# Kernel tuning notes

Hardware: AMD Instinct MI355X
Metric: run time of the kernel (lower is better)

Reference implementation:

```python
import jax, jax.numpy as jnp
import numpy as np

N = 6000
E = 192000
H = 128
NUM_HEADS = 4

def _segsum(x, idx, n):
    return jax.ops.segment_sum(x, idx, num_segments=n)

def _gcn_encode(x, edges, W0, b0, Ws, bs):
    n = x.shape[0]
    sl = jnp.arange(n, dtype=edges.dtype)
    row = jnp.concatenate([edges[0], sl])  # source
    col = jnp.concatenate([edges[1], sl])  # target (aggregation)
    deg = _segsum(jnp.ones_like(col, dtype=x.dtype), col, n)
    dinv = jax.lax.rsqrt(deg)  # deg >= 1 thanks to self loops
    norm = (dinv[row] * dinv[col])[:, None]
    def layer(h, W, b):
        hw = h @ W
        agg = _segsum(hw[row] * norm, col, n)
        return jax.nn.relu(agg + b)
    h = layer(x, W0, b0)
    for i in range(Ws.shape[0]):
        h = layer(h, Ws[i], bs[i])
    return h

def setup_inputs() -> dict:
    key = jax.random.key(0)
    ks = jax.random.split(key, 24)
    def lin(k, fan_in, shape):
        return jax.random.normal(k, shape, dtype=jnp.float32) / np.sqrt(fan_in)
    return {
        'x_resting': jax.random.normal(ks[0], (N, 3), dtype=jnp.float32),
        'x_rigid': jax.random.normal(ks[1], (N, 3), dtype=jnp.float32),
        'edge_resting': jax.random.randint(ks[2], (2, E), 0, N, dtype=jnp.int32),
        'edge_rigid': jax.random.randint(ks[3], (2, E), 0, N, dtype=jnp.int32),
        'Wr0': lin(ks[4], 3, (3, H)), 'br0': jnp.zeros((H,), jnp.float32),
        'Wr': lin(ks[5], H, (2, H, H)), 'br': jnp.zeros((2, H), jnp.float32),
        'Wg0': lin(ks[6], 3, (3, H)), 'bg0': jnp.zeros((H,), jnp.float32),
        'Wg': lin(ks[7], H, (2, H, H)), 'bg': jnp.zeros((2, H), jnp.float32),
        'Wa': lin(ks[8], H, (NUM_HEADS, H, H)), 'ba': jnp.zeros((NUM_HEADS, H), jnp.float32),
        'Wd0': lin(ks[9], H * (NUM_HEADS + 1), (H * (NUM_HEADS + 1), H)), 'bd0': jnp.zeros((H,), jnp.float32),
        'Wd': lin(ks[10], H, (2, H, H)), 'bd': jnp.zeros((2, H), jnp.float32),
        'Wout': lin(ks[11], H, (H, 3)), 'bout': jnp.zeros((3,), jnp.float32),
    }

def reference(x_resting, x_rigid, edge_resting, edge_rigid,
              Wr0, br0, Wr, br, Wg0, bg0, Wg, bg,
              Wa, ba, Wd0, bd0, Wd, bd, Wout, bout):
    xr = _gcn_encode(x_resting, edge_resting, Wr0, br0, Wr, br)  # (N,H)
    xg = _gcn_encode(x_rigid, edge_rigid, Wg0, bg0, Wg, bg)      # (N,H)

    def head(W, b):
        q = xr @ W + b            # (N,H)
        k = xg @ W + b            # (N,H)
        attn = jax.nn.softmax(q @ k.T, axis=-1)  # (N,N) dense per head
        return attn @ xg          # (N,H)
    heads = jax.vmap(head)(Wa, ba)                       # (heads,N,H)
    pooled = heads.transpose(1, 0, 2).reshape(xr.shape[0], -1)  # (N, heads*H)

    h = jnp.concatenate([xr, pooled], axis=-1)  # (N, H*(heads+1))
    h = jax.nn.relu(h @ Wd0 + bd0)
    for i in range(Wd.shape[0]):
        h = jax.nn.relu(h @ Wd[i] + bd[i])
    return h @ Wout + bout  # (N, 3) deformed positions
```

## Files before the change

kernel.cpp:

```cpp
#include <hip/hip_runtime.h>
#include <math.h>

#define N_NODES 6000
#define N_EDGES 192000
#define H 128
#define NHEADS 4
#define HCAT 640
#define NPAD 6016
#define NTILES 188

typedef unsigned short ushort_t;
typedef __attribute__((ext_vector_type(8))) short short8;
typedef __attribute__((ext_vector_type(16))) float f32x16;

__device__ __forceinline__ void bf16split(float x, ushort_t& hi, ushort_t& lo) {
    unsigned ub = __float_as_uint(x);
    unsigned hb = ub & 0xffff0000u;
    float l = x - __uint_as_float(hb);
    hi = (ushort_t)(hb >> 16);
    lo = (ushort_t)(__float_as_uint(l) >> 16);
}

__device__ __forceinline__ void gll16(const ushort_t* g, ushort_t* l) {
    __builtin_amdgcn_global_load_lds((const __attribute__((address_space(1))) void*)g,
                                     (__attribute__((address_space(3))) void*)l, 16, 0, 0);
}

__global__ void zero_ints(int* p, int n) {
    int i = blockIdx.x * 256 + threadIdx.x;
    if (i < n) p[i] = 0;
}

__global__ void hist2(const int* __restrict__ eA, const int* __restrict__ eB,
                      int* __restrict__ cnt) {
    int e = blockIdx.x * 256 + threadIdx.x;
    int z = blockIdx.y;
    const int* edges = z ? eB : eA;
    if (e < N_EDGES) atomicAdd(&cnt[z * N_NODES + edges[N_EDGES + e]], 1);
}

__global__ __launch_bounds__(1024)
void scan2(const int* __restrict__ cnt_all, int* __restrict__ rs_all,
           float* __restrict__ dinv_all) {
    __shared__ int ps[1024];
    int z = blockIdx.x;
    const int* cnt = cnt_all + z * N_NODES;
    int* row_start = rs_all + z * (N_NODES + 1);
    float* dinv = dinv_all + z * N_NODES;
    int t = threadIdx.x;
    int base = t * 6;
    int local[6];
    int s = 0;
#pragma unroll
    for (int j = 0; j < 6; ++j) {
        int idx = base + j;
        int v = (idx < N_NODES) ? cnt[idx] : 0;
        local[j] = s;
        s += v;
        if (idx < N_NODES) dinv[idx] = rsqrtf((float)(v + 1));
    }
    ps[t] = s;
    __syncthreads();
    for (int off = 1; off < 1024; off <<= 1) {
        int v = (t >= off) ? ps[t - off] : 0;
        __syncthreads();
        ps[t] += v;
        __syncthreads();
    }
    int ex = (t > 0) ? ps[t - 1] : 0;
#pragma unroll
    for (int j = 0; j < 6; ++j) {
        int idx = base + j;
        if (idx < N_NODES) row_start[idx] = ex + local[j];
    }
    if (t == 1023) row_start[N_NODES] = ps[1023];
}

__global__ void place2(const int* __restrict__ eA, const int* __restrict__ eB,
                       const int* __restrict__ rs_all, int* __restrict__ cur_all,
                       int* __restrict__ eslot_all) {
    int e = blockIdx.x * 256 + threadIdx.x;
    int z = blockIdx.y;
    const int* edges = z ? eB : eA;
    if (e < N_EDGES) {
        int tg = edges[N_EDGES + e];
        int p = atomicAdd(&cur_all[z * N_NODES + tg], 1);
        eslot_all[(size_t)z * N_EDGES + rs_all[z * (N_NODES + 1) + tg] + p] = e;
    }
}

__global__ __launch_bounds__(256)
void gather_x3(const float* __restrict__ xA, const float* __restrict__ xB,
               const int* __restrict__ eA, const int* __restrict__ eB,
               const int* __restrict__ eslot_all, const int* __restrict__ rs_all,
               const float* __restrict__ dinv_all,
               float* __restrict__ outA, float* __restrict__ outB) {
    int z = blockIdx.y;
    int n = blockIdx.x * 256 + threadIdx.x;
    if (n >= N_NODES) return;
    const int* edges = z ? eB : eA;
    const int* eslot = eslot_all + (size_t)z * N_EDGES;
    const int* row_start = rs_all + z * (N_NODES + 1);
    const float* x = z ? xB : xA;
    const float* dv = dinv_all + z * N_NODES;
    float* out = z ? outB : outA;
    float di = dv[n];
    float a0 = x[n * 3 + 0] * di * di;
    float a1 = x[n * 3 + 1] * di * di;
    float a2 = x[n * 3 + 2] * di * di;
    int s0 = row_start[n], s1 = row_start[n + 1];
    for (int i = s0; i < s1; ++i) {
        int e = eslot[i];
        int s = edges[e];
        float nr = dv[s] * di;
        a0 += x[s * 3 + 0] * nr;
        a1 += x[s * 3 + 1] * nr;
        a2 += x[s * 3 + 2] * nr;
    }
    out[n * 3 + 0] = a0; out[n * 3 + 1] = a1; out[n * 3 + 2] = a2;
}

__global__ __launch_bounds__(256)
void gcn_gemm2(const float* __restrict__ hinA, const float* __restrict__ hinB,
               const float* __restrict__ WA, const float* __restrict__ WB,
               float* __restrict__ hwA, float* __restrict__ hwB, int in_dim,
               const float* __restrict__ bA, const float* __restrict__ bB, int do_relu) {
    __shared__ float xs[16 * H];
    int z = blockIdx.y;
    const float* hin = z ? hinB : hinA;
    const float* W = z ? WB : WA;
    float* hw = z ? hwB : hwA;
    const float* b = z ? bB : bA;
    int n0 = blockIdx.x * 16;
    int t = threadIdx.x;
    int f = t & (H - 1);
    int g = t >> 7;
    for (int i = t; i < 16 * H; i += 256) {
        int r = i >> 7, c = i & (H - 1);
        xs[i] = (c < in_dim) ? hin[(size_t)(n0 + r) * in_dim + c] : 0.f;
    }
    __syncthreads();
    float acc[8];
#pragma unroll
    for (int j = 0; j < 8; ++j) acc[j] = 0.f;
    for (int d = 0; d < in_dim; ++d) {
        float w = W[d * H + f];
#pragma unroll
        for (int j = 0; j < 8; ++j) acc[j] += xs[(g * 8 + j) * H + d] * w;
    }
    if (do_relu) {
        float bias = b[f];
#pragma unroll
        for (int j = 0; j < 8; ++j)
            hw[(size_t)(n0 + g * 8 + j) * H + f] = fmaxf(acc[j] + bias, 0.f);
    } else {
#pragma unroll
        for (int j = 0; j < 8; ++j) hw[(size_t)(n0 + g * 8 + j) * H + f] = acc[j];
    }
}

__global__ __launch_bounds__(H)
void gather2(const int* __restrict__ eA, const int* __restrict__ eB,
             const int* __restrict__ eslot_all, const int* __restrict__ rs_all,
             const float* __restrict__ hwA, const float* __restrict__ hwB,
             const float* __restrict__ dinv_all,
             const float* __restrict__ bA, const float* __restrict__ bB,
             float* __restrict__ outA, float* __restrict__ outB, int osA, int osB) {
    __shared__ int ssrc[128];
    __shared__ float snrm[128];
    int z = blockIdx.y;
    const int* edges = z ? eB : eA;
    const int* eslot = eslot_all + (size_t)z * N_EDGES;
    const int* row_start = rs_all + z * (N_NODES + 1);
    const float* hw = z ? hwB : hwA;
    const float* dinv = dinv_all + z * N_NODES;
    const float* b = z ? bB : bA;
    float* out = z ? outB : outA;
    int ostride = z ? osB : osA;

    int tg = blockIdx.x, f = threadIdx.x;
    int s0 = row_start[tg], s1 = row_start[tg + 1];
    float di = dinv[tg];
    float acc = hw[(size_t)tg * H + f] * di * di;
    for (int base = s0; base < s1; base += 128) {
        int cnt = min(128, s1 - base);
        __syncthreads();
        if (f < cnt) {
            int e = eslot[base + f];
            int s = edges[e];
            ssrc[f] = s;
            snrm[f] = dinv[s] * di;
        }
        __syncthreads();
        for (int i = 0; i < cnt; ++i)
            acc += hw[(size_t)ssrc[i] * H + f] * snrm[i];
    }
    float v = acc + b[f];
    out[(size_t)tg * ostride + f] = v > 0.f ? v : 0.f;
}

__global__ __launch_bounds__(256)
void qk_kernel2(const float* __restrict__ qs, int qstride, const float* __restrict__ xg,
                const float* __restrict__ Wa, const float* __restrict__ ba,
                ushort_t* __restrict__ Qh, ushort_t* __restrict__ Ql,
                ushort_t* __restrict__ Khs, ushort_t* __restrict__ Kls) {
    __shared__ float xs[2][16][H];
    int n0 = blockIdx.x * 16, head = blockIdx.y;
    int t = threadIdx.x;
    int f = t & (H - 1);
    int g = t >> 7;
    for (int i = t; i < 2 * 16 * H; i += 256) {
        int which = i >> 11;
        int rem = i & 2047;
        int row = rem >> 7, col = rem & 127;
        xs[which][row][col] = which ? xg[(size_t)(n0 + row) * H + col]
                                    : qs[(size_t)(n0 + row) * qstride + col];
    }
    __syncthreads();
    const float* W = Wa + (size_t)head * H * H;
    float bias = ba[head * H + f];
    float acc[16];
#pragma unroll
    for (int j = 0; j < 16; ++j) acc[j] = bias;
    for (int d = 0; d < H; ++d) {
        float w = W[d * H + f];
#pragma unroll
        for (int j = 0; j < 16; ++j) acc[j] += xs[g][j][d] * w;
    }
#pragma unroll
    for (int j = 0; j < 16; ++j) {
        int n = n0 + j;
        ushort_t hi, lo;
        bf16split(acc[j], hi, lo);
        if (g == 0) {
            size_t idx = ((size_t)(head * N_NODES + n) << 7) + f;
            Qh[idx] = hi; Ql[idx] = lo;
        } else {
            int pos = (((f >> 3) ^ (n & 15)) << 3) + (f & 7);
            size_t idx = ((size_t)(head * NPAD + n) << 7) + pos;
            Khs[idx] = hi; Kls[idx] = lo;
        }
    }
}

__global__ void zero_pad_k(ushort_t* __restrict__ Khs, ushort_t* __restrict__ Kls) {
    int i = blockIdx.x * 256 + threadIdx.x;
    if (i < NHEADS * 16 * H) {
        int head = i / (16 * H);
        int rest = i - head * 16 * H;
        int n = N_NODES + (rest >> 7);
        int f = rest & 127;
        size_t idx = ((size_t)(head * NPAD + n) << 7) + f;
        Khs[idx] = 0; Kls[idx] = 0;
    }
}

__global__ __launch_bounds__(128)
void cvt_vt(const float* __restrict__ xg, ushort_t* __restrict__ Vth, ushort_t* __restrict__ Vtl) {
    __shared__ float vs[32][129];
    int t0 = blockIdx.x;
    int t = threadIdx.x;
    for (int c = t; c < 32 * 32; c += 128) {
        int row = c >> 5, col4 = (c & 31) << 2;
        int n = t0 * 32 + row;
        float4 v = (n < N_NODES) ? *(const float4*)&xg[(size_t)n * H + col4]
                                 : float4{0.f, 0.f, 0.f, 0.f};
        vs[row][col4 + 0] = v.x; vs[row][col4 + 1] = v.y;
        vs[row][col4 + 2] = v.z; vs[row][col4 + 3] = v.w;
    }
    __syncthreads();
    int d = t;
    size_t base = ((size_t)t0 * H + d) * 32;
#pragma unroll
    for (int oc = 0; oc < 4; ++oc) {
        int cc = oc ^ (d & 3);
        unsigned uh[4], ul[4];
#pragma unroll
        for (int j = 0; j < 4; ++j) {
            ushort_t h0, l0, h1, l1;
            bf16split(vs[cc * 8 + 2 * j][d], h0, l0);
            bf16split(vs[cc * 8 + 2 * j + 1][d], h1, l1);
            uh[j] = (unsigned)h0 | ((unsigned)h1 << 16);
            ul[j] = (unsigned)l0 | ((unsigned)l1 << 16);
        }
        *(uint4*)&Vth[base + oc * 8] = make_uint4(uh[0], uh[1], uh[2], uh[3]);
        *(uint4*)&Vtl[base + oc * 8] = make_uint4(ul[0], ul[1], ul[2], ul[3]);
    }
}

__global__ __launch_bounds__(256, 2)
void attn_mfma7(const ushort_t* __restrict__ Qh, const ushort_t* __restrict__ Ql,
                const ushort_t* __restrict__ Khs, const ushort_t* __restrict__ Kls,
                const ushort_t* __restrict__ Vth, const ushort_t* __restrict__ Vtl,
                float* __restrict__ Opart, float* __restrict__ mlpart, int tps) {
    __shared__ ushort_t lds[2][4][4096];
    const int head = blockIdx.y;
    const int sp = blockIdx.z;
    const int t = threadIdx.x;
    const int lane = t & 63;
    const int w = t >> 6;
    const int r = lane & 31;
    const int h = lane >> 5;
    const int q0w = blockIdx.x * 128 + w * 32;

    int t_begin = sp * tps;
    int t_end = t_begin + tps; if (t_end > NTILES) t_end = NTILES;

    const size_t kbase = (size_t)head * NPAD * H;
    const int o1 = t * 8, o2 = t * 8 + 2048;

    int qr = q0w + r; if (qr > N_NODES - 1) qr = N_NODES - 1;
    const size_t qbase = ((size_t)(head * N_NODES + qr)) << 7;
    short8 qfh[8], qfl[8];
#pragma unroll
    for (int s = 0; s < 8; ++s) {
        qfh[s] = *(const short8*)&Qh[qbase + 16 * s + 8 * h];
        qfl[s] = *(const short8*)&Ql[qbase + 16 * s + 8 * h];
    }

    f32x16 O[4];
#pragma unroll
    for (int sub = 0; sub < 4; ++sub)
#pragma unroll
        for (int i = 0; i < 16; ++i) O[sub][i] = 0.f;
    float mrun = -1e30f, lrun = 0.f;
    short8 aPh[2], aPl[2];
    float alpha_prev = 1.f;
    int resc_prev = 0;

    {
        const ushort_t* sKh = Khs + kbase + (size_t)t_begin * 4096;
        const ushort_t* sKl = Kls + kbase + (size_t)t_begin * 4096;
        gll16(sKh + o1, &lds[0][0][o1]); gll16(sKh + o2, &lds[0][0][o2]);
        gll16(sKl + o1, &lds[0][1][o1]); gll16(sKl + o2, &lds[0][1][o2]);
    }

    for (int it = t_begin; it < t_end; ++it) {
        const int b = (it - t_begin) & 1;
        __syncthreads();
        {
            int nt = it + 1; if (nt >= t_end) nt = t_begin;
            const ushort_t* sKh = Khs + kbase + (size_t)nt * 4096;
            const ushort_t* sKl = Kls + kbase + (size_t)nt * 4096;
            const ushort_t* sVh = Vth + (size_t)it * 4096;
            const ushort_t* sVl = Vtl + (size_t)it * 4096;
            gll16(sKh + o1, &lds[b ^ 1][0][o1]); gll16(sKh + o2, &lds[b ^ 1][0][o2]);
            gll16(sKl + o1, &lds[b ^ 1][1][o1]); gll16(sKl + o2, &lds[b ^ 1][1][o2]);
            gll16(sVh + o1, &lds[b ^ 1][2][o1]); gll16(sVh + o2, &lds[b ^ 1][2][o2]);
            gll16(sVl + o1, &lds[b ^ 1][3][o1]); gll16(sVl + o2, &lds[b ^ 1][3][o2]);
        }
        const ushort_t* lKh = &lds[b][0][0];
        const ushort_t* lKl = &lds[b][1][0];
        const ushort_t* lVh = &lds[b][2][0];
        const ushort_t* lVl = &lds[b][3][0];

        f32x16 acc;
#pragma unroll
        for (int i = 0; i < 16; ++i) acc[i] = 0.f;
        const int krow = r * H;
#pragma unroll
        for (int s = 0; s < 8; ++s) {
            int cc = ((2 * s + h) ^ (r & 15)) << 3;
            short8 ah = *(const short8*)&lKh[krow + cc];
            short8 al = *(const short8*)&lKl[krow + cc];
            acc = __builtin_amdgcn_mfma_f32_32x32x16_bf16(ah, qfh[s], acc, 0, 0, 0);
            acc = __builtin_amdgcn_mfma_f32_32x32x16_bf16(ah, qfl[s], acc, 0, 0, 0);
            acc = __builtin_amdgcn_mfma_f32_32x32x16_bf16(al, qfh[s], acc, 0, 0, 0);
        }

        if (it != t_begin) {
            if (resc_prev) {
#pragma unroll
                for (int i = 0; i < 16; ++i) {
                    int rowq = (i & 3) + 8 * (i >> 2) + 4 * h;
                    float a = __shfl(alpha_prev, rowq);
#pragma unroll
                    for (int sub = 0; sub < 4; ++sub) O[sub][i] *= a;
                }
            }
#pragma unroll
            for (int sub = 0; sub < 4; ++sub) {
                const int vrow = (32 * sub + r) * 32;
#pragma unroll
                for (int s2 = 0; s2 < 2; ++s2) {
                    int cc = (((2 * s2 + h) ^ (r & 3)) << 3);
                    short8 bh = *(const short8*)&lVh[vrow + cc];
                    short8 bl = *(const short8*)&lVl[vrow + cc];
                    O[sub] = __builtin_amdgcn_mfma_f32_32x32x16_bf16(aPh[s2], bh, O[sub], 0, 0, 0);
                    O[sub] = __builtin_amdgcn_mfma_f32_32x32x16_bf16(aPh[s2], bl, O[sub], 0, 0, 0);
                    O[sub] = __builtin_amdgcn_mfma_f32_32x32x16_bf16(aPl[s2], bh, O[sub], 0, 0, 0);
                }
            }
        }

        float sv[16];
#pragma unroll
        for (int i = 0; i < 16; ++i) sv[i] = acc[i];
        int klim = N_NODES - (it << 5);
        if (klim < 32) {
#pragma unroll
            for (int i = 0; i < 16; ++i) {
                int row = (i & 3) + 8 * (i >> 2) + 4 * h;
                if (row >= klim) sv[i] = -1e30f;
            }
        }
        float tmax = sv[0];
#pragma unroll
        for (int i = 1; i < 16; ++i) tmax = fmaxf(tmax, sv[i]);
        tmax = fmaxf(tmax, __shfl_xor(tmax, 32));
        float mnew = fmaxf(mrun, tmax);
        float p[16];
        float psum = 0.f;
#pragma unroll
        for (int i = 0; i < 16; ++i) { p[i] = __expf(sv[i] - mnew); psum += p[i]; }

        if (__ballot(mnew > mrun)) {
            float alpha = __expf(mrun - mnew);
            lrun *= alpha;
            alpha_prev = alpha;
            resc_prev = 1;
        } else {
            resc_prev = 0;
        }
        lrun += psum;
        mrun = mnew;

        float pr[16];
#pragma unroll
        for (int i = 0; i < 16; ++i) pr[i] = __shfl_xor(p[i], 32);
#pragma unroll
        for (int s2 = 0; s2 < 2; ++s2) {
#pragma unroll
            for (int j = 0; j < 8; ++j) {
                int c = j & 3;
                float v;
                if (j < 4) v = (h == 0) ? p[c + 8 * s2] : pr[c + 8 * s2 + 4];
                else       v = (h == 1) ? p[c + 8 * s2 + 4] : pr[c + 8 * s2];
                unsigned ub = __float_as_uint(v);
                unsigned hb = ub & 0xffff0000u;
                float lo = v - __uint_as_float(hb);
                aPh[s2][j] = (short)(hb >> 16);
                aPl[s2][j] = (short)(__float_as_uint(lo) >> 16);
            }
        }
    }

    __syncthreads();
    {
        const int bl = (t_end - t_begin) & 1;
        const ushort_t* lVh = &lds[bl][2][0];
        const ushort_t* lVl = &lds[bl][3][0];
        if (resc_prev) {
#pragma unroll
            for (int i = 0; i < 16; ++i) {
                int rowq = (i & 3) + 8 * (i >> 2) + 4 * h;
                float a = __shfl(alpha_prev, rowq);
#pragma unroll
                for (int sub = 0; sub < 4; ++sub) O[sub][i] *= a;
            }
        }
#pragma unroll
        for (int sub = 0; sub < 4; ++sub) {
            const int vrow = (32 * sub + r) * 32;
#pragma unroll
            for (int s2 = 0; s2 < 2; ++s2) {
                int cc = (((2 * s2 + h) ^ (r & 3)) << 3);
                short8 bh = *(const short8*)&lVh[vrow + cc];
                short8 bl = *(const short8*)&lVl[vrow + cc];
                O[sub] = __builtin_amdgcn_mfma_f32_32x32x16_bf16(aPh[s2], bh, O[sub], 0, 0, 0);
                O[sub] = __builtin_amdgcn_mfma_f32_32x32x16_bf16(aPh[s2], bl, O[sub], 0, 0, 0);
                O[sub] = __builtin_amdgcn_mfma_f32_32x32x16_bf16(aPl[s2], bh, O[sub], 0, 0, 0);
            }
        }
    }

    lrun += __shfl_xor(lrun, 32);

    float* Ob = Opart + (size_t)(sp * NHEADS + head) * NPAD * H;
#pragma unroll
    for (int i = 0; i < 16; ++i) {
        int rowq = (i & 3) + 8 * (i >> 2) + 4 * h;
        int qg = q0w + rowq;
        if (qg < N_NODES) {
            float* dst = &Ob[(size_t)qg * H + r];
#pragma unroll
            for (int sub = 0; sub < 4; ++sub) dst[32 * sub] = O[sub][i];
        }
    }
    if (h == 0 && q0w + r < N_NODES) {
        float2* ml = (float2*)mlpart;
        ml[(size_t)(sp * NHEADS + head) * NPAD + q0w + r] = make_float2(mrun, lrun);
    }
}

__global__ __launch_bounds__(256)
void attn_combine(const float* __restrict__ Opart, const float* __restrict__ mlpart,
                  float* __restrict__ hcat, int ns) {
    int idx = blockIdx.x * 256 + threadIdx.x;
    if (idx >= NHEADS * N_NODES * (H / 4)) return;
    int head = idx / (N_NODES * (H / 4));
    int rest = idx - head * N_NODES * (H / 4);
    int q = rest >> 5;
    int d4 = (rest & 31) << 2;
    const float2* ml = (const float2*)mlpart;
    float m = -1e30f;
    for (int s = 0; s < ns; ++s)
        m = fmaxf(m, ml[(size_t)(s * NHEADS + head) * NPAD + q].x);
    float lsum = 0.f;
    float4 o = {0.f, 0.f, 0.f, 0.f};
    for (int s = 0; s < ns; ++s) {
        float2 v = ml[(size_t)(s * NHEADS + head) * NPAD + q];
        float wgt = __expf(v.x - m);
        lsum += v.y * wgt;
        float4 ov = *(const float4*)&Opart[((size_t)(s * NHEADS + head) * NPAD + q) * H + d4];
        o.x += ov.x * wgt; o.y += ov.y * wgt; o.z += ov.z * wgt; o.w += ov.w * wgt;
    }
    float inv = 1.f / lsum;
    float4 res = {o.x * inv, o.y * inv, o.z * inv, o.w * inv};
    *(float4*)&hcat[(size_t)q * HCAT + H + head * H + d4] = res;
}

__global__ __launch_bounds__(256)
void decoder(const float* __restrict__ hcat,
             const float* __restrict__ Wd0, const float* __restrict__ bd0,
             const float* __restrict__ Wd, const float* __restrict__ bd,
             const float* __restrict__ Wout, const float* __restrict__ bout,
             float* __restrict__ out) {
    __shared__ float s0[8 * HCAT];
    __shared__ float s1[8 * H];
    __shared__ float s2[8 * H];
    int n0 = blockIdx.x * 8;
    int t = threadIdx.x;
    int f = t & (H - 1);
    int g = t >> 7;
    for (int i = t; i < 8 * HCAT; i += 256)
        s0[i] = hcat[(size_t)n0 * HCAT + i];
    __syncthreads();

    float acc[4];
#pragma unroll
    for (int j = 0; j < 4; ++j) acc[j] = bd0[f];
    for (int d = 0; d < HCAT; ++d) {
        float w = Wd0[d * H + f];
#pragma unroll
        for (int j = 0; j < 4; ++j) acc[j] += s0[(g * 4 + j) * HCAT + d] * w;
    }
#pragma unroll
    for (int j = 0; j < 4; ++j) s1[(g * 4 + j) * H + f] = fmaxf(acc[j], 0.f);
    __syncthreads();

#pragma unroll
    for (int j = 0; j < 4; ++j) acc[j] = bd[f];
    for (int d = 0; d < H; ++d) {
        float w = Wd[d * H + f];
#pragma unroll
        for (int j = 0; j < 4; ++j) acc[j] += s1[(g * 4 + j) * H + d] * w;
    }
#pragma unroll
    for (int j = 0; j < 4; ++j) s2[(g * 4 + j) * H + f] = fmaxf(acc[j], 0.f);
    __syncthreads();

#pragma unroll
    for (int j = 0; j < 4; ++j) acc[j] = bd[H + f];
    for (int d = 0; d < H; ++d) {
        float w = Wd[H * H + d * H + f];
#pragma unroll
        for (int j = 0; j < 4; ++j) acc[j] += s2[(g * 4 + j) * H + d] * w;
    }
    __syncthreads();
#pragma unroll
    for (int j = 0; j < 4; ++j) s1[(g * 4 + j) * H + f] = fmaxf(acc[j], 0.f);
    __syncthreads();

    if (t < 24) {
        int n = t / 3, c = t % 3;
        float o = bout[c];
        for (int d = 0; d < H; ++d) o += s1[n * H + d] * Wout[d * 3 + c];
        out[(size_t)(n0 + n) * 3 + c] = o;
    }
}

extern "C" void kernel_launch(void* const* d_in, const int* in_sizes, int n_in,
                              void* d_out, int out_size, void* d_ws, size_t ws_size,
                              hipStream_t stream) {
    const float* x_rest = (const float*)d_in[0];
    const float* x_rig  = (const float*)d_in[1];
    const int*   e_rest = (const int*)d_in[2];
    const int*   e_rig  = (const int*)d_in[3];
    const float* Wr0 = (const float*)d_in[4];
    const float* br0 = (const float*)d_in[5];
    const float* Wr  = (const float*)d_in[6];
    const float* br  = (const float*)d_in[7];
    const float* Wg0 = (const float*)d_in[8];
    const float* bg0 = (const float*)d_in[9];
    const float* Wg  = (const float*)d_in[10];
    const float* bg  = (const float*)d_in[11];
    const float* Wa  = (const float*)d_in[12];
    const float* ba  = (const float*)d_in[13];
    const float* Wd0 = (const float*)d_in[14];
    const float* bd0 = (const float*)d_in[15];
    const float* Wd  = (const float*)d_in[16];
    const float* bd  = (const float*)d_in[17];
    const float* Wout = (const float*)d_in[18];
    const float* bout = (const float*)d_in[19];
    float* out = (float*)d_out;

    const size_t NH = (size_t)N_NODES * H;
    float* ws = (float*)d_ws;
    float* dinv = ws;
    float* hw   = dinv + 2 * N_NODES;
    float* hb   = hw + 2 * NH;
    float* hcat = hb + 2 * NH;
    float* ha   = hcat;
    float* xg   = hb + NH;
    float* xagg = hb;
    ushort_t* Qh  = (ushort_t*)(hcat + (size_t)N_NODES * HCAT);
    ushort_t* Ql  = Qh + (size_t)NHEADS * N_NODES * H;
    ushort_t* Khs = Ql + (size_t)NHEADS * N_NODES * H;
    ushort_t* Kls = Khs + (size_t)NHEADS * NPAD * H;
    ushort_t* Vth = Kls + (size_t)NHEADS * NPAD * H;
    ushort_t* Vtl = Vth + (size_t)NTILES * H * 32;
    int* ib   = (int*)(Vtl + (size_t)NTILES * H * 32);
    int* cnt  = ib;
    int* cur  = cnt + 2 * N_NODES;
    int* rs   = cur + 2 * N_NODES;
    int* eslot = rs + 2 * (N_NODES + 1);
    int* iend  = eslot + 2 * N_EDGES;
    float* Opart = (float*)(((uintptr_t)iend + 15) & ~(uintptr_t)15);

    size_t base_bytes = (size_t)((char*)Opart - (char*)d_ws);
    size_t per_split  = (size_t)NHEADS * NPAD * (H + 2) * sizeof(float);
    int NS = 2;
    if (ws_size >= base_bytes + 5 * per_split + (1u << 20)) NS = 5;
    else if (ws_size >= base_bytes + 4 * per_split + (1u << 20)) NS = 4;
    float* mlpart = Opart + (size_t)NS * NHEADS * NPAD * H;
    int tps = (NTILES + NS - 1) / NS;

    const int gN = (N_NODES + 255) / 256;
    const int gE = (N_EDGES + 255) / 256;

    zero_ints<<<(4 * N_NODES + 255) / 256, 256, 0, stream>>>(cnt, 4 * N_NODES);
    hist2<<<dim3(gE, 2), 256, 0, stream>>>(e_rest, e_rig, cnt);
    scan2<<<2, 1024, 0, stream>>>(cnt, rs, dinv);
    place2<<<dim3(gE, 2), 256, 0, stream>>>(e_rest, e_rig, rs, cur, eslot);

    float* hw_r = hw, * hw_g = hw + NH;
    float* ha_r = ha, * ha_g = ha + NH;
    float* hb_r = hb, * hb_g = hb + NH;
    float* xagg_r = xagg, * xagg_g = xagg + 3 * N_NODES;

    gather_x3<<<dim3(gN, 2), 256, 0, stream>>>(x_rest, x_rig, e_rest, e_rig, eslot, rs,
                                               dinv, xagg_r, xagg_g);
    gcn_gemm2<<<dim3(N_NODES / 16, 2), 256, 0, stream>>>(xagg_r, xagg_g, Wr0, Wg0,
                                                         ha_r, ha_g, 3, br0, bg0, 1);
    gcn_gemm2<<<dim3(N_NODES / 16, 2), 256, 0, stream>>>(ha_r, ha_g, Wr, Wg, hw_r, hw_g, H,
                                                         nullptr, nullptr, 0);
    gather2<<<dim3(N_NODES, 2), H, 0, stream>>>(e_rest, e_rig, eslot, rs, hw_r, hw_g, dinv,
                                                br, bg, hb_r, hb_g, H, H);
    gcn_gemm2<<<dim3(N_NODES / 16, 2), 256, 0, stream>>>(hb_r, hb_g, Wr + H * H, Wg + H * H,
                                                         hw_r, hw_g, H, nullptr, nullptr, 0);
    gather2<<<dim3(N_NODES, 2), H, 0, stream>>>(e_rest, e_rig, eslot, rs, hw_r, hw_g, dinv,
                                                br + H, bg + H, hcat, xg, HCAT, H);

    qk_kernel2<<<dim3(N_NODES / 16, NHEADS), 256, 0, stream>>>(hcat, HCAT, xg, Wa, ba,
                                                               Qh, Ql, Khs, Kls);
    zero_pad_k<<<(NHEADS * 16 * H + 255) / 256, 256, 0, stream>>>(Khs, Kls);
    cvt_vt<<<NTILES, 128, 0, stream>>>(xg, Vth, Vtl);
    attn_mfma7<<<dim3(47, NHEADS, NS), 256, 0, stream>>>(Qh, Ql, Khs, Kls, Vth, Vtl,
                                                         Opart, mlpart, tps);
    attn_combine<<<(NHEADS * N_NODES * (H / 4) + 255) / 256, 256, 0, stream>>>(Opart, mlpart,
                                                                               hcat, NS);

    decoder<<<N_NODES / 8, 256, 0, stream>>>(hcat, Wd0, bd0, Wd, bd, Wout, bout, out);
}
```

Before: 610.9 us.

## Fuse first GCN layer, merge attention prep kernels, restructure attention loop scheduling

Fuses the first-layer feature gather with its 3-wide linear projection, using 16 threads per node plus a shuffle reduction, which removes two launches and an intermediate buffer. Merges the Q/K projection, V transpose/convert and K padding zeroing into one attn_prep launch dispatched by block index. The attention kernel now prefetches V with K in the prologue and performs the PV MFMA unconditionally (P is zero-initialised). Rescaling is moved to the top of the loop, the P cross-lane exchange is cut to 8 shuffles, and sched_group_barrier hints interleave MFMA, DS reads and VALU work. The aim is fewer launches and better MFMA/LDS overlap in the attention loop, at the cost of more complex scheduling that could regress.

```diff
diff --git a/kernel.cpp b/kernel.cpp
--- a/kernel.cpp
+++ b/kernel.cpp
@@ -90,26 +90,31 @@
 }
 
 __global__ __launch_bounds__(256)
-void gather_x3(const float* __restrict__ xA, const float* __restrict__ xB,
-               const int* __restrict__ eA, const int* __restrict__ eB,
-               const int* __restrict__ eslot_all, const int* __restrict__ rs_all,
-               const float* __restrict__ dinv_all,
-               float* __restrict__ outA, float* __restrict__ outB) {
+void l1_fused(const float* __restrict__ xA, const float* __restrict__ xB,
+              const int* __restrict__ eA, const int* __restrict__ eB,
+              const int* __restrict__ eslot_all, const int* __restrict__ rs_all,
+              const float* __restrict__ dinv_all,
+              const float* __restrict__ WA, const float* __restrict__ WB,
+              const float* __restrict__ bA, const float* __restrict__ bB,
+              float* __restrict__ outA, float* __restrict__ outB) {
+    __shared__ float xs[16][4];
     int z = blockIdx.y;
-    int n = blockIdx.x * 256 + threadIdx.x;
-    if (n >= N_NODES) return;
     const int* edges = z ? eB : eA;
     const int* eslot = eslot_all + (size_t)z * N_EDGES;
     const int* row_start = rs_all + z * (N_NODES + 1);
     const float* x = z ? xB : xA;
     const float* dv = dinv_all + z * N_NODES;
+    const float* W = z ? WB : WA;
+    const float* bb = z ? bB : bA;
     float* out = z ? outB : outA;
+    int n0 = blockIdx.x * 16;
+    int t = threadIdx.x;
+    int ln = t >> 4, slot = t & 15;
+    int n = n0 + ln;
     float di = dv[n];
-    float a0 = x[n * 3 + 0] * di * di;
-    float a1 = x[n * 3 + 1] * di * di;
-    float a2 = x[n * 3 + 2] * di * di;
+    float a0 = 0.f, a1 = 0.f, a2 = 0.f;
     int s0 = row_start[n], s1 = row_start[n + 1];
-    for (int i = s0; i < s1; ++i) {
+    for (int i = s0 + slot; i < s1; i += 16) {
         int e = eslot[i];
         int s = edges[e];
         float nr = dv[s] * di;
@@ -117,46 +122,55 @@
         a1 += x[s * 3 + 1] * nr;
         a2 += x[s * 3 + 2] * nr;
     }
-    out[n * 3 + 0] = a0; out[n * 3 + 1] = a1; out[n * 3 + 2] = a2;
+#pragma unroll
+    for (int off = 1; off < 16; off <<= 1) {
+        a0 += __shfl_xor(a0, off);
+        a1 += __shfl_xor(a1, off);
+        a2 += __shfl_xor(a2, off);
+    }
+    if (slot == 0) {
+        xs[ln][0] = a0 + x[n * 3 + 0] * di * di;
+        xs[ln][1] = a1 + x[n * 3 + 1] * di * di;
+        xs[ln][2] = a2 + x[n * 3 + 2] * di * di;
+    }
+    __syncthreads();
+    int f = t & 127, g = t >> 7;
+    float bias = bb[f];
+    float w0 = W[0 * H + f], w1 = W[1 * H + f], w2 = W[2 * H + f];
+#pragma unroll
+    for (int j = 0; j < 8; ++j) {
+        int node = g * 8 + j;
+        float acc = bias + xs[node][0] * w0 + xs[node][1] * w1 + xs[node][2] * w2;
+        out[(size_t)(n0 + node) * H + f] = fmaxf(acc, 0.f);
+    }
 }
 
 __global__ __launch_bounds__(256)
 void gcn_gemm2(const float* __restrict__ hinA, const float* __restrict__ hinB,
                const float* __restrict__ WA, const float* __restrict__ WB,
-               float* __restrict__ hwA, float* __restrict__ hwB, int in_dim,
-               const float* __restrict__ bA, const float* __restrict__ bB, int do_relu) {
+               float* __restrict__ hwA, float* __restrict__ hwB) {
     __shared__ float xs[16 * H];
     int z = blockIdx.y;
     const float* hin = z ? hinB : hinA;
     const float* W = z ? WB : WA;
     float* hw = z ? hwB : hwA;
-    const float* b = z ? bB : bA;
     int n0 = blockIdx.x * 16;
     int t = threadIdx.x;
     int f = t & (H - 1);
     int g = t >> 7;
-    for (int i = t; i < 16 * H; i += 256) {
-        int r = i >> 7, c = i & (H - 1);
-        xs[i] = (c < in_dim) ? hin[(size_t)(n0 + r) * in_dim + c] : 0.f;
-    }
+    for (int i = t; i < 16 * H; i += 256)
+        xs[i] = hin[(size_t)n0 * H + i];
     __syncthreads();
     float acc[8];
 #pragma unroll
     for (int j = 0; j < 8; ++j) acc[j] = 0.f;
-    for (int d = 0; d < in_dim; ++d) {
+    for (int d = 0; d < H; ++d) {
         float w = W[d * H + f];
 #pragma unroll
         for (int j = 0; j < 8; ++j) acc[j] += xs[(g * 8 + j) * H + d] * w;
     }
-    if (do_relu) {
-        float bias = b[f];
-#pragma unroll
-        for (int j = 0; j < 8; ++j)
-            hw[(size_t)(n0 + g * 8 + j) * H + f] = fmaxf(acc[j] + bias, 0.f);
-    } else {
-#pragma unroll
-        for (int j = 0; j < 8; ++j) hw[(size_t)(n0 + g * 8 + j) * H + f] = acc[j];
-    }
+#pragma unroll
+    for (int j = 0; j < 8; ++j) hw[(size_t)(n0 + g * 8 + j) * H + f] = acc[j];
 }
 
 __global__ __launch_bounds__(H)
@@ -200,99 +214,101 @@
 }
 
 __global__ __launch_bounds__(256)
-void qk_kernel2(const float* __restrict__ qs, int qstride, const float* __restrict__ xg,
-                const float* __restrict__ Wa, const float* __restrict__ ba,
-                ushort_t* __restrict__ Qh, ushort_t* __restrict__ Ql,
-                ushort_t* __restrict__ Khs, ushort_t* __restrict__ Kls) {
-    __shared__ float xs[2][16][H];
-    int n0 = blockIdx.x * 16, head = blockIdx.y;
+void attn_prep(const float* __restrict__ qs, const float* __restrict__ xg,
+               const float* __restrict__ Wa, const float* __restrict__ ba,
+               ushort_t* __restrict__ Qh, ushort_t* __restrict__ Ql,
+               ushort_t* __restrict__ Khs, ushort_t* __restrict__ Kls,
+               ushort_t* __restrict__ Vth, ushort_t* __restrict__ Vtl) {
+    __shared__ float smem[4224];
+    int bx = blockIdx.x;
     int t = threadIdx.x;
-    int f = t & (H - 1);
-    int g = t >> 7;
-    for (int i = t; i < 2 * 16 * H; i += 256) {
-        int which = i >> 11;
-        int rem = i & 2047;
-        int row = rem >> 7, col = rem & 127;
-        xs[which][row][col] = which ? xg[(size_t)(n0 + row) * H + col]
-                                    : qs[(size_t)(n0 + row) * qstride + col];
-    }
-    __syncthreads();
-    const float* W = Wa + (size_t)head * H * H;
-    float bias = ba[head * H + f];
-    float acc[16];
-#pragma unroll
-    for (int j = 0; j < 16; ++j) acc[j] = bias;
-    for (int d = 0; d < H; ++d) {
-        float w = W[d * H + f];
-#pragma unroll
-        for (int j = 0; j < 16; ++j) acc[j] += xs[g][j][d] * w;
-    }
-#pragma unroll
-    for (int j = 0; j < 16; ++j) {
-        int n = n0 + j;
-        ushort_t hi, lo;
-        bf16split(acc[j], hi, lo);
-        if (g == 0) {
-            size_t idx = ((size_t)(head * N_NODES + n) << 7) + f;
-            Qh[idx] = hi; Ql[idx] = lo;
-        } else {
-            int pos = (((f >> 3) ^ (n & 15)) << 3) + (f & 7);
-            size_t idx = ((size_t)(head * NPAD + n) << 7) + pos;
-            Khs[idx] = hi; Kls[idx] = lo;
-        }
-    }
-}
-
-__global__ void zero_pad_k(ushort_t* __restrict__ Khs, ushort_t* __restrict__ Kls) {
-    int i = blockIdx.x * 256 + threadIdx.x;
-    if (i < NHEADS * 16 * H) {
-        int head = i / (16 * H);
-        int rest = i - head * 16 * H;
-        int n = N_NODES + (rest >> 7);
-        int f = rest & 127;
-        size_t idx = ((size_t)(head * NPAD + n) << 7) + f;
-        Khs[idx] = 0; Kls[idx] = 0;
-    }
-}
-
-__global__ __launch_bounds__(128)
-void cvt_vt(const float* __restrict__ xg, ushort_t* __restrict__ Vth, ushort_t* __restrict__ Vtl) {
-    __shared__ float vs[32][129];
-    int t0 = blockIdx.x;
-    int t = threadIdx.x;
-    for (int c = t; c < 32 * 32; c += 128) {
-        int row = c >> 5, col4 = (c & 31) << 2;
-        int n = t0 * 32 + row;
-        float4 v = (n < N_NODES) ? *(const float4*)&xg[(size_t)n * H + col4]
-                                 : float4{0.f, 0.f, 0.f, 0.f};
-        vs[row][col4 + 0] = v.x; vs[row][col4 + 1] = v.y;
-        vs[row][col4 + 2] = v.z; vs[row][col4 + 3] = v.w;
-    }
-    __syncthreads();
-    int d = t;
-    size_t base = ((size_t)t0 * H + d) * 32;
-#pragma unroll
-    for (int oc = 0; oc < 4; ++oc) {
-        int cc = oc ^ (d & 3);
-        unsigned uh[4], ul[4];
-#pragma unroll
-        for (int j = 0; j < 4; ++j) {
-            ushort_t h0, l0, h1, l1;
-            bf16split(vs[cc * 8 + 2 * j][d], h0, l0);
-            bf16split(vs[cc * 8 + 2 * j + 1][d], h1, l1);
-            uh[j] = (unsigned)h0 | ((unsigned)h1 << 16);
-            ul[j] = (unsigned)l0 | ((unsigned)l1 << 16);
-        }
-        *(uint4*)&Vth[base + oc * 8] = make_uint4(uh[0], uh[1], uh[2], uh[3]);
-        *(uint4*)&Vtl[base + oc * 8] = make_uint4(ul[0], ul[1], ul[2], ul[3]);
+    if (bx < 1500) {
+        int head = bx / 375;
+        int n0 = (bx - head * 375) * 16;
+        float* xs = smem;
+        int f = t & (H - 1);
+        int g = t >> 7;
+        for (int i = t; i < 2 * 16 * H; i += 256) {
+            int which = i >> 11;
+            int rem = i & 2047;
+            int row = rem >> 7, col = rem & 127;
+            xs[i] = which ? xg[(size_t)(n0 + row) * H + col]
+                          : qs[(size_t)(n0 + row) * HCAT + col];
+        }
+        __syncthreads();
+        const float* W = Wa + (size_t)head * H * H;
+        float bias = ba[head * H + f];
+        float acc[16];
+#pragma unroll
+        for (int j = 0; j < 16; ++j) acc[j] = bias;
+        for (int d = 0; d < H; ++d) {
+            float w = W[d * H + f];
+#pragma unroll
+            for (int j = 0; j < 16; ++j) acc[j] += xs[g * 2048 + j * H + d] * w;
+        }
+#pragma unroll
+        for (int j = 0; j < 16; ++j) {
+            int n = n0 + j;
+            ushort_t hi, lo;
+            bf16split(acc[j], hi, lo);
+            if (g == 0) {
+                size_t idx = ((size_t)(head * N_NODES + n) << 7) + f;
+                Qh[idx] = hi; Ql[idx] = lo;
+            } else {
+                int pos = (((f >> 3) ^ (n & 15)) << 3) + (f & 7);
+                size_t idx = ((size_t)(head * NPAD + n) << 7) + pos;
+                Khs[idx] = hi; Kls[idx] = lo;
+            }
+        }
+    } else if (bx < 1688) {
+        int t0 = bx - 1500;
+        float (*vs)[129] = (float(*)[129])smem;
+        for (int c = t; c < 32 * 32; c += 256) {
+            int row = c >> 5, col4 = (c & 31) << 2;
+            int n = t0 * 32 + row;
+            float4 v = (n < N_NODES) ? *(const float4*)&xg[(size_t)n * H + col4]
+                                     : float4{0.f, 0.f, 0.f, 0.f};
+            vs[row][col4 + 0] = v.x; vs[row][col4 + 1] = v.y;
+            vs[row][col4 + 2] = v.z; vs[row][col4 + 3] = v.w;
+        }
+        __syncthreads();
+        int d = t & 127;
+        int ocb = (t >> 7) * 2;
+        size_t base = ((size_t)t0 * H + d) * 32;
+#pragma unroll
+        for (int oo = 0; oo < 2; ++oo) {
+            int oc = ocb + oo;
+            int cc = oc ^ (d & 3);
+            unsigned uh[4], ul[4];
+#pragma unroll
+            for (int j = 0; j < 4; ++j) {
+                ushort_t h0, l0, h1, l1;
+                bf16split(vs[cc * 8 + 2 * j][d], h0, l0);
+                bf16split(vs[cc * 8 + 2 * j + 1][d], h1, l1);
+                uh[j] = (unsigned)h0 | ((unsigned)h1 << 16);
+                ul[j] = (unsigned)l0 | ((unsigned)l1 << 16);
+            }
+            *(uint4*)&Vth[base + oc * 8] = make_uint4(uh[0], uh[1], uh[2], uh[3]);
+            *(uint4*)&Vtl[base + oc * 8] = make_uint4(ul[0], ul[1], ul[2], ul[3]);
+        }
+    } else {
+        int i = (bx - 1688) * 256 + t;
+        if (i < NHEADS * 16 * H) {
+            int head = i / (16 * H);
+            int rest = i - head * 16 * H;
+            int n = N_NODES + (rest >> 7);
+            int f = rest & 127;
+            size_t idx = ((size_t)(head * NPAD + n) << 7) + f;
+            Khs[idx] = 0; Kls[idx] = 0;
+        }
     }
 }
 
 __global__ __launch_bounds__(256, 2)
-void attn_mfma7(const ushort_t* __restrict__ Qh, const ushort_t* __restrict__ Ql,
-                const ushort_t* __restrict__ Khs, const ushort_t* __restrict__ Kls,
-                const ushort_t* __restrict__ Vth, const ushort_t* __restrict__ Vtl,
-                float* __restrict__ Opart, float* __restrict__ mlpart, int tps) {
+void attn_mfma10(const ushort_t* __restrict__ Qh, const ushort_t* __restrict__ Ql,
+                 const ushort_t* __restrict__ Khs, const ushort_t* __restrict__ Kls,
+                 const ushort_t* __restrict__ Vth, const ushort_t* __restrict__ Vtl,
+                 float* __restrict__ Opart, float* __restrict__ mlpart, int tps) {
     __shared__ ushort_t lds[2][4][4096];
     const int head = blockIdx.y;
     const int sp = blockIdx.z;
@@ -325,19 +341,38 @@
         for (int i = 0; i < 16; ++i) O[sub][i] = 0.f;
     float mrun = -1e30f, lrun = 0.f;
     short8 aPh[2], aPl[2];
+#pragma unroll
+    for (int s2 = 0; s2 < 2; ++s2)
+#pragma unroll
+        for (int j = 0; j < 8; ++j) { aPh[s2][j] = 0; aPl[s2][j] = 0; }
     float alpha_prev = 1.f;
     int resc_prev = 0;
 
     {
         const ushort_t* sKh = Khs + kbase + (size_t)t_begin * 4096;
         const ushort_t* sKl = Kls + kbase + (size_t)t_begin * 4096;
+        const ushort_t* sVh = Vth + (size_t)t_begin * 4096;
+        const ushort_t* sVl = Vtl + (size_t)t_begin * 4096;
         gll16(sKh + o1, &lds[0][0][o1]); gll16(sKh + o2, &lds[0][0][o2]);
         gll16(sKl + o1, &lds[0][1][o1]); gll16(sKl + o2, &lds[0][1][o2]);
+        gll16(sVh + o1, &lds[0][2][o1]); gll16(sVh + o2, &lds[0][2][o2]);
+        gll16(sVl + o1, &lds[0][3][o1]); gll16(sVl + o2, &lds[0][3][o2]);
     }
 
     for (int it = t_begin; it < t_end; ++it) {
         const int b = (it - t_begin) & 1;
         __syncthreads();
+
+        if (resc_prev) {
+#pragma unroll
+            for (int i = 0; i < 16; ++i) {
+                int rowq = (i & 3) + 8 * (i >> 2) + 4 * h;
+                float a = __shfl(alpha_prev, rowq);
+#pragma unroll
+                for (int sub = 0; sub < 4; ++sub) O[sub][i] *= a;
+            }
+        }
+
         {
             int nt = it + 1; if (nt >= t_end) nt = t_begin;
             const ushort_t* sKh = Khs + kbase + (size_t)nt * 4096;
@@ -368,80 +403,77 @@
             acc = __builtin_amdgcn_mfma_f32_32x32x16_bf16(al, qfh[s], acc, 0, 0, 0);
         }
 
-        if (it != t_begin) {
-            if (resc_prev) {
-#pragma unroll
-                for (int i = 0; i < 16; ++i) {
-                    int rowq = (i & 3) + 8 * (i >> 2) + 4 * h;
-                    float a = __shfl(alpha_prev, rowq);
-#pragma unroll
-                    for (int sub = 0; sub < 4; ++sub) O[sub][i] *= a;
-                }
+#pragma unroll
+        for (int sub = 0; sub < 4; ++sub) {
+            const int vrow = (32 * sub + r) * 32;
+#pragma unroll
+            for (int s2 = 0; s2 < 2; ++s2) {
+                int cc = (((2 * s2 + h) ^ (r & 3)) << 3);
+                short8 bh = *(const short8*)&lVh[vrow + cc];
+                short8 bl = *(const short8*)&lVl[vrow + cc];
+                O[sub] = __builtin_amdgcn_mfma_f32_32x32x16_bf16(aPh[s2], bh, O[sub], 0, 0, 0);
+                O[sub] = __builtin_amdgcn_mfma_f32_32x32x16_bf16(aPh[s2], bl, O[sub], 0, 0, 0);
+                O[sub] = __builtin_amdgcn_mfma_f32_32x32x16_bf16(aPl[s2], bh, O[sub], 0, 0, 0);
             }
-#pragma unroll
-            for (int sub = 0; sub < 4; ++sub) {
-                const int vrow = (32 * sub + r) * 32;
-#pragma unroll
-                for (int s2 = 0; s2 < 2; ++s2) {
-                    int cc = (((2 * s2 + h) ^ (r & 3)) << 3);
-                    short8 bh = *(const short8*)&lVh[vrow + cc];
-                    short8 bl = *(const short8*)&lVl[vrow + cc];
-                    O[sub] = __builtin_amdgcn_mfma_f32_32x32x16_bf16(aPh[s2], bh, O[sub], 0, 0, 0);
-                    O[sub] = __builtin_amdgcn_mfma_f32_32x32x16_bf16(aPh[s2], bl, O[sub], 0, 0, 0);
-                    O[sub] = __builtin_amdgcn_mfma_f32_32x32x16_bf16(aPl[s2], bh, O[sub], 0, 0, 0);
-                }
-            }
-        }
-
+        }
+
+        int klim = N_NODES - (it << 5);
         float sv[16];
 #pragma unroll
-        for (int i = 0; i < 16; ++i) sv[i] = acc[i];
-        int klim = N_NODES - (it << 5);
-        if (klim < 32) {
-#pragma unroll
-            for (int i = 0; i < 16; ++i) {
-                int row = (i & 3) + 8 * (i >> 2) + 4 * h;
-                if (row >= klim) sv[i] = -1e30f;
-            }
+        for (int i = 0; i < 16; ++i) {
+            int row = (i & 3) + 8 * (i >> 2) + 4 * h;
+            sv[i] = (row < klim) ? acc[i] : -1e30f;
         }
         float tmax = sv[0];
 #pragma unroll
         for (int i = 1; i < 16; ++i) tmax = fmaxf(tmax, sv[i]);
         tmax = fmaxf(tmax, __shfl_xor(tmax, 32));
         float mnew = fmaxf(mrun, tmax);
+        float alpha = __expf(mrun - mnew);
+        resc_prev = (__ballot(mnew > mrun) != 0ull) ? 1 : 0;
+        alpha_prev = alpha;
         float p[16];
         float psum = 0.f;
 #pragma unroll
         for (int i = 0; i < 16; ++i) { p[i] = __expf(sv[i] - mnew); psum += p[i]; }
-
-        if (__ballot(mnew > mrun)) {
-            float alpha = __expf(mrun - mnew);
-            lrun *= alpha;
-            alpha_prev = alpha;
-            resc_prev = 1;
-        } else {
-            resc_prev = 0;
-        }
-        lrun += psum;
+        lrun = lrun * alpha + psum;
         mrun = mnew;
 
-        float pr[16];
-#pragma unroll
-        for (int i = 0; i < 16; ++i) pr[i] = __shfl_xor(p[i], 32);
+        float tmp[8], rv[8];
+#pragma unroll
+        for (int k = 0; k < 8; ++k) {
+            int i0 = (k & 3) + 8 * (k >> 2);
+            tmp[k] = h ? p[i0] : p[i0 + 4];
+        }
+#pragma unroll
+        for (int k = 0; k < 8; ++k) rv[k] = __shfl_xor(tmp[k], 32);
 #pragma unroll
         for (int s2 = 0; s2 < 2; ++s2) {
 #pragma unroll
             for (int j = 0; j < 8; ++j) {
                 int c = j & 3;
                 float v;
-                if (j < 4) v = (h == 0) ? p[c + 8 * s2] : pr[c + 8 * s2 + 4];
-                else       v = (h == 1) ? p[c + 8 * s2 + 4] : pr[c + 8 * s2];
+                if (j < 4) v = (h == 0) ? p[c + 8 * s2] : rv[c + 4 * s2];
+                else       v = (h == 1) ? p[c + 8 * s2 + 4] : rv[c + 4 * s2];
                 unsigned ub = __float_as_uint(v);
                 unsigned hb = ub & 0xffff0000u;
                 float lo = v - __uint_as_float(hb);
                 aPh[s2][j] = (short)(hb >> 16);
                 aPl[s2][j] = (short)(__float_as_uint(lo) >> 16);
             }
+        }
+
+        __builtin_amdgcn_sched_group_barrier(0x010, 16, 0);
+#pragma unroll
+        for (int g2 = 0; g2 < 8; ++g2) {
+            __builtin_amdgcn_sched_group_barrier(0x100, 2, 0);
+            __builtin_amdgcn_sched_group_barrier(0x008, 3, 0);
+        }
+#pragma unroll
+        for (int g2 = 0; g2 < 8; ++g2) {
+            __builtin_amdgcn_sched_group_barrier(0x100, 2, 0);
+            __builtin_amdgcn_sched_group_barrier(0x008, 3, 0);
+            __builtin_amdgcn_sched_group_barrier(0x002, 14, 0);
         }
     }
 
@@ -613,7 +645,6 @@
     float* hcat = hb + 2 * NH;
     float* ha   = hcat;
     float* xg   = hb + NH;
-    float* xagg = hb;
     ushort_t* Qh  = (ushort_t*)(hcat + (size_t)N_NODES * HCAT);
     ushort_t* Ql  = Qh + (size_t)NHEADS * N_NODES * H;
     ushort_t* Khs = Ql + (size_t)NHEADS * N_NODES * H;
@@ -636,7 +667,6 @@
     float* mlpart = Opart + (size_t)NS * NHEADS * NPAD * H;
     int tps = (NTILES + NS - 1) / NS;
 
-    const int gN = (N_NODES + 255) / 256;
     const int gE = (N_EDGES + 255) / 256;
 
     zero_ints<<<(4 * N_NODES + 255) / 256, 256, 0, stream>>>(cnt, 4 * N_NODES);
@@ -647,27 +677,21 @@
     float* hw_r = hw, * hw_g = hw + NH;
     float* ha_r = ha, * ha_g = ha + NH;
     float* hb_r = hb, * hb_g = hb + NH;
-    float* xagg_r = xagg, * xagg_g = xagg + 3 * N_NODES;
-
-    gather_x3<<<dim3(gN, 2), 256, 0, stream>>>(x_rest, x_rig, e_rest, e_rig, eslot, rs,
-                                               dinv, xagg_r, xagg_g);
-    gcn_gemm2<<<dim3(N_NODES / 16, 2), 256, 0, stream>>>(xagg_r, xagg_g, Wr0, Wg0,
-                                                         ha_r, ha_g, 3, br0, bg0, 1);
-    gcn_gemm2<<<dim3(N_NODES / 16, 2), 256, 0, stream>>>(ha_r, ha_g, Wr, Wg, hw_r, hw_g, H,
-                                                         nullptr, nullptr, 0);
+
+    l1_fused<<<dim3(N_NODES / 16, 2), 256, 0, stream>>>(x_rest, x_rig, e_rest, e_rig,
+                                                        eslot, rs, dinv, Wr0, Wg0,
+                                                        br0, bg0, ha_r, ha_g);
+    gcn_gemm2<<<dim3(N_NODES / 16, 2), 256, 0, stream>>>(ha_r, ha_g, Wr, Wg, hw_r, hw_g);
     gather2<<<dim3(N_NODES, 2), H, 0, stream>>>(e_rest, e_rig, eslot, rs, hw_r, hw_g, dinv,
                                                 br, bg, hb_r, hb_g, H, H);
     gcn_gemm2<<<dim3(N_NODES / 16, 2), 256, 0, stream>>>(hb_r, hb_g, Wr + H * H, Wg + H * H,
-                                                         hw_r, hw_g, H, nullptr, nullptr, 0);
+                                                         hw_r, hw_g);
     gather2<<<dim3(N_NODES, 2), H, 0, stream>>>(e_rest, e_rig, eslot, rs, hw_r, hw_g, dinv,
                                                 br + H, bg + H, hcat, xg, HCAT, H);
 
-    qk_kernel2<<<dim3(N_NODES / 16, NHEADS), 256, 0, stream>>>(hcat, HCAT, xg, Wa, ba,
-                                                               Qh, Ql, Khs, Kls);
-    zero_pad_k<<<(NHEADS * 16 * H + 255) / 256, 256, 0, stream>>>(Khs, Kls);
-    cvt_vt<<<NTILES, 128, 0, stream>>>(xg, Vth, Vtl);
-    attn_mfma7<<<dim3(47, NHEADS, NS), 256, 0, stream>>>(Qh, Ql, Khs, Kls, Vth, Vtl,
-                                                         Opart, mlpart, tps);
+    attn_prep<<<1720, 256, 0, stream>>>(hcat, xg, Wa, ba, Qh, Ql, Khs, Kls, Vth, Vtl);
+    attn_mfma10<<<dim3(47, NHEADS, NS), 256, 0, stream>>>(Qh, Ql, Khs, Kls, Vth, Vtl,
+                                                          Opart, mlpart, tps);
     attn_combine<<<(NHEADS * N_NODES * (H / 4) + 255) / 256, 256, 0, stream>>>(Opart, mlpart,
                                                                                hcat, NS);
 
```

Measured after the change: 569.7 us. -6.7%, faster.
